# Optimization experiments

Hardware: AMD Instinct MI355X
Metric: run time of the kernel (lower is better)

Reference implementation:

```python
import jax, jax.numpy as jnp
import numpy as np

N_NODES = 100000
N_EDGES = 1000000
F_IN = 32       # CFG.feature_dim
H = 64          # CFG.hidden_dim
H2 = 2 * H      # L1 family: conv1 out = hidden_dim * 2
N_GRAPHS = 64


def gcn_conv(x, src, dst, deg_inv_sqrt, W, b, num_nodes):
    # PyG GCNConv: out = D^{-1/2} (A + I) D^{-1/2} (x @ W) + b
    h = x @ W  # [N, out]
    norm = (deg_inv_sqrt[src] * deg_inv_sqrt[dst])[:, None]  # [E+N, 1]
    msg = h[src] * norm
    return jax.ops.segment_sum(msg, dst, num_segments=num_nodes) + b


def setup_inputs() -> dict:
    key = jax.random.key(0)
    ks = jax.random.split(key, 10)
    x = jax.random.normal(ks[0], (N_NODES, F_IN), dtype=jnp.float32)
    edge_index = jax.random.randint(ks[1], (2, N_EDGES), 0, N_NODES, dtype=jnp.int64)
    batch = jnp.sort(jax.random.randint(ks[2], (N_NODES,), 0, N_GRAPHS, dtype=jnp.int64))
    def glorot(k, shape):
        lim = np.sqrt(6.0 / (shape[0] + shape[1]))
        return jax.random.uniform(k, shape, jnp.float32, -lim, lim)
    W1 = glorot(ks[3], (F_IN, H2))
    b1 = jnp.zeros((H2,), jnp.float32)
    W2 = glorot(ks[4], (H2, H))
    b2 = jnp.zeros((H,), jnp.float32)
    Wrt = glorot(ks[5], (H, H))
    brt = jnp.zeros((H,), jnp.float32)
    return {"x": x, "edge_index": edge_index, "batch": batch,
            "W1": W1, "b1": b1, "W2": W2, "b2": b2, "Wrt": Wrt, "brt": brt}


def reference(x, edge_index, batch, W1, b1, W2, b2, Wrt, brt):
    num_nodes = x.shape[0]
    loop = jnp.arange(num_nodes, dtype=edge_index.dtype)
    src = jnp.concatenate([edge_index[0], loop])  # add self-loops
    dst = jnp.concatenate([edge_index[1], loop])
    deg = jax.ops.segment_sum(jnp.ones_like(dst, dtype=x.dtype), dst, num_segments=num_nodes)
    deg_inv_sqrt = jnp.where(deg > 0, jax.lax.rsqrt(deg), 0.0)

    h = jax.nn.relu(gcn_conv(x, src, dst, deg_inv_sqrt, W1, b1, num_nodes))
    h = gcn_conv(h, src, dst, deg_inv_sqrt, W2, b2, num_nodes)
    h = h @ Wrt + brt  # L1 reverse transcriptase

    # global_mean_pool over batch segments
    sums = jax.ops.segment_sum(h, batch, num_segments=N_GRAPHS)
    counts = jax.ops.segment_sum(jnp.ones((num_nodes,), h.dtype), batch, num_segments=N_GRAPHS)
    pooled = sums / jnp.maximum(counts, 1.0)[:, None]

    activity_factor = 1.0  # age = 0 -> 1/(1+0)
    return pooled * activity_factor
```

## Files before the change

### kernel.cpp

```cpp
#include <hip/hip_runtime.h>

#define NN 100000
#define NE 1000000
#define FIN 32
#define H2 128
#define HH 64
#define NG 64
#define SLOT 16
#define OSLOT 48

#define BSH 9
#define BNODES 512
#define NB 196
#define CAPL 28
#define CAPB 6144
#define CHUNK 2048
#define NSPILL 4096
#define ZN (NN + NG + NG * HH + 256 + 64)

typedef __attribute__((ext_vector_type(8))) short short8;
typedef __attribute__((ext_vector_type(4))) float f32x4;
typedef __attribute__((ext_vector_type(2))) float f32x2;

__device__ __forceinline__ unsigned f2bf(float f) {
    unsigned u = __float_as_uint(f);
    return (u + 0x7FFFu + ((u >> 16) & 1u)) >> 16;
}
__device__ __forceinline__ float bf2f(unsigned u) {
    return __uint_as_float(u << 16);
}
__device__ __forceinline__ void dec8(float* a, float w, uint2 v) {
    f32x2 p0 = __builtin_amdgcn_cvt_pk_f32_fp8((int)v.x, false);
    f32x2 p1 = __builtin_amdgcn_cvt_pk_f32_fp8((int)v.x, true);
    f32x2 p2 = __builtin_amdgcn_cvt_pk_f32_fp8((int)v.y, false);
    f32x2 p3 = __builtin_amdgcn_cvt_pk_f32_fp8((int)v.y, true);
    a[0] = fmaf(w, p0.x, a[0]); a[1] = fmaf(w, p0.y, a[1]);
    a[2] = fmaf(w, p1.x, a[2]); a[3] = fmaf(w, p1.y, a[3]);
    a[4] = fmaf(w, p2.x, a[4]); a[5] = fmaf(w, p2.y, a[5]);
    a[6] = fmaf(w, p3.x, a[6]); a[7] = fmaf(w, p3.y, a[7]);
}
__device__ __forceinline__ unsigned char f2fp8(float f) {
    return (unsigned char)(__builtin_amdgcn_cvt_pk_fp8_f32(f, f, 0, false) & 0xff);
}

__global__ void k_setup(const float* __restrict__ x, const float* __restrict__ W1,
                        const float* __restrict__ W2, const float* __restrict__ Wrt,
                        const float* __restrict__ b2, const float* __restrict__ brt,
                        int* __restrict__ zws, uint2* __restrict__ xb8,
                        unsigned short* __restrict__ w2t, float* __restrict__ brt2,
                        unsigned short* __restrict__ w1t) {
    int i = blockIdx.x * 256 + threadIdx.x;
    if (i < ZN) zws[i] = 0;
    if (i < NN * FIN / 8) {
        float4 a = ((const float4*)x)[2 * i];
        float4 b = ((const float4*)x)[2 * i + 1];
        unsigned u0 = __builtin_amdgcn_cvt_pk_fp8_f32(a.x, a.y, 0, false);
        u0 = __builtin_amdgcn_cvt_pk_fp8_f32(a.z, a.w, u0, true);
        unsigned u1 = __builtin_amdgcn_cvt_pk_fp8_f32(b.x, b.y, 0, false);
        u1 = __builtin_amdgcn_cvt_pk_fp8_f32(b.z, b.w, u1, true);
        xb8[i] = make_uint2(u0, u1);
    }
    if (i < H2 * HH) {
        int r = i >> 6, c = i & 63;
        float acc = 0.f;
        for (int k = 0; k < HH; ++k) acc = fmaf(W2[r * HH + k], Wrt[k * HH + c], acc);
        w2t[c * H2 + r] = (unsigned short)f2bf(acc);
    } else if (i < H2 * HH + HH) {
        int c = i - H2 * HH;
        float acc = brt[c];
        for (int k = 0; k < HH; ++k) acc = fmaf(b2[k], Wrt[k * HH + c], acc);
        brt2[c] = acc;
    } else if (i < H2 * HH + HH + FIN * H2) {
        int j = i - (H2 * HH + HH);
        int k = j >> 7, c = j & 127;
        w1t[c * FIN + k] = (unsigned short)f2bf(W1[j]);
    }
}

__global__ __launch_bounds__(256) void k_bin(const int* __restrict__ ei,
                                             int* __restrict__ gcnt,
                                             unsigned* __restrict__ gbuf,
                                             int* __restrict__ gspillc,
                                             int* __restrict__ gspill) {
    __shared__ int cur[NB];
    __shared__ int gbase[NB];
    __shared__ unsigned stage[NB * CAPL];
    for (int i = threadIdx.x; i < NB; i += 256) cur[i] = 0;
    __syncthreads();
    int e0 = blockIdx.x * CHUNK;
#pragma unroll
    for (int it = 0; it < CHUNK / 256; ++it) {
        int e = e0 + it * 256 + threadIdx.x;
        if (e < NE) {
            int d = ei[NE + e];
            int b = d >> BSH;
            unsigned u = ((unsigned)ei[e] << BSH) | (unsigned)(d & (BNODES - 1));
            int p = atomicAdd(&cur[b], 1);
            if (p < CAPL) stage[b * CAPL + p] = u;
            else {
                int q = atomicAdd(gspillc, 1);
                if (q < NSPILL) { gspill[2 * q] = b; gspill[2 * q + 1] = (int)u; }
            }
        }
    }
    __syncthreads();
    if (threadIdx.x < NB) {
        int len = min(cur[threadIdx.x], CAPL);
        gbase[threadIdx.x] = len ? atomicAdd(&gcnt[threadIdx.x], len) : 0;
    }
    __syncthreads();
    int wid = threadIdx.x >> 6, lane = threadIdx.x & 63;
    for (int b = wid; b < NB; b += 4) {
        int len = min(cur[b], CAPL);
        if (len == 0) continue;
        int base = gbase[b];
        if (base + len > CAPB) len = max(0, CAPB - base);
        if (lane < len)
            gbuf[(size_t)b * CAPB + base + lane] = stage[b * CAPL + lane];
    }
}

__global__ __launch_bounds__(512) void k_build(const unsigned* __restrict__ gbuf,
                                               const int* __restrict__ gcnt,
                                               const int* __restrict__ gspillc,
                                               const int* __restrict__ gspill,
                                               const int* __restrict__ bat,
                                               int* __restrict__ esrc,
                                               int* __restrict__ ovf,
                                               int* __restrict__ fill,
                                               float* __restrict__ dis,
                                               int* __restrict__ counts) {
    __shared__ int cnt[BNODES];
    __shared__ int slots[BNODES * SLOT];
    for (int i = threadIdx.x; i < BNODES; i += 512) cnt[i] = 0;
    __syncthreads();
    int b = blockIdx.x;
    int len = min(gcnt[b], CAPB);
    const unsigned* buf = gbuf + (size_t)b * CAPB;
    for (int i = threadIdx.x; i < len; i += 512) {
        unsigned u = buf[i];
        int ln = u & (BNODES - 1);
        int src = (int)(u >> BSH);
        int p = atomicAdd(&cnt[ln], 1);
        if (p < SLOT) slots[ln * SLOT + p] = src;
        else if (p < SLOT + OSLOT)
            ovf[(size_t)(b * BNODES + ln) * OSLOT + (p - SLOT)] = src;
    }
    int ns = min(*gspillc, NSPILL);
    for (int i = threadIdx.x; i < ns; i += 512) {
        if (gspill[2 * i] == b) {
            unsigned u = (unsigned)gspill[2 * i + 1];
            int ln = u & (BNODES - 1);
            int src = (int)(u >> BSH);
            int p = atomicAdd(&cnt[ln], 1);
            if (p < SLOT) slots[ln * SLOT + p] = src;
            else if (p < SLOT + OSLOT)
                ovf[(size_t)(b * BNODES + ln) * OSLOT + (p - SLOT)] = src;
        }
    }
    __syncthreads();
    int nbase = b * BNODES;
    int nvalid = min(BNODES, NN - nbase);
    if (nvalid <= 0) return;
    {
        int li = threadIdx.x;
        bool v = li < nvalid;
        int n = nbase + li;
        if (v) {
            int c = cnt[li];
            fill[n] = c;
            dis[n] = rsqrtf((float)(c + 1));
        }
        int lane = li & 63;
        int g = v ? bat[n] : -1;
        int gprev = __shfl_up(g, 1, 64);
        bool head = (lane == 0) || (g != gprev);
        unsigned long long hm = __ballot(head && v);
        int gnext = __shfl_down(g, 1, 64);
        bool tail = v && ((lane == 63) || (gnext != g));
        if (tail) {
            unsigned long long below =
                (lane == 63) ? ~0ull : ((1ull << (lane + 1)) - 1ull);
            int start = 63 - __clzll(hm & below);
            atomicAdd(&counts[g], lane - start + 1);
        }
    }
    int nwords = nvalid * SLOT / 4;
    int4* d4 = (int4*)(esrc + (size_t)nbase * SLOT);
    const int4* s4 = (const int4*)slots;
    for (int i = threadIdx.x; i < nwords; i += 512) d4[i] = s4[i];
}

__global__ void k_pack(const int* __restrict__ cnt, const float* __restrict__ dis,
                       int* __restrict__ esrc, int* __restrict__ ovf) {
    int i = blockIdx.x * 256 + threadIdx.x;
    if (i < NN * SLOT) {
        int n = i >> 4, p = i & 15;
        if (p < min(cnt[n], SLOT)) {
            int s = esrc[i];
            esrc[i] = (int)(((unsigned)s << 15) | (f2bf(dis[s]) & 0x7FFFu));
        }
    } else if (i < NN * SLOT + NN) {
        int n = i - NN * SLOT;
        int c = cnt[n];
        if (c > SLOT) {
            int cov = min(c - SLOT, OSLOT);
            int* orow = ovf + (size_t)n * OSLOT;
            for (int q = 0; q < cov; ++q) {
                int s = orow[q];
                orow[q] = (int)(((unsigned)s << 15) | (f2bf(dis[s]) & 0x7FFFu));
            }
        }
    }
}

__global__ __launch_bounds__(256, 4) void k_aggx(
    const uint2* __restrict__ xb8, const float* __restrict__ dis,
    const int* __restrict__ cnt, const int* __restrict__ esrc,
    const int* __restrict__ ovf, uint4* __restrict__ aggx4) {
    int idx = blockIdx.x * 256 + threadIdx.x;
    int n = idx >> 2, t = idx & 3;
    if (n >= NN) return;
    float dn = dis[n];
    float a[8] = {0.f, 0.f, 0.f, 0.f, 0.f, 0.f, 0.f, 0.f};
    dec8(a, dn * dn, xb8[n * 4 + t]);
    int c = cnt[n];
    int c1 = min(c, SLOT);
    if (c1 > 0) {
        const int4* rp = (const int4*)(esrc + (size_t)n * SLOT);
        int4 i0 = rp[0], i1 = rp[1], i2 = rp[2], i3 = rp[3];
        int ej[16] = {i0.x, i0.y, i0.z, i0.w, i1.x, i1.y, i1.z, i1.w,
                      i2.x, i2.y, i2.z, i2.w, i3.x, i3.y, i3.z, i3.w};
        int e0 = i0.x;
#pragma unroll
        for (int j = 0; j < 16; ++j) {
            int e = (j < c1) ? ej[j] : e0;
            int s = (int)((unsigned)e >> 15);
            float w = (j < c1) ? bf2f(e & 0x7FFF) * dn : 0.f;
            dec8(a, w, xb8[(size_t)s * 4 + t]);
        }
    }
    if (c > SLOT) {
        int cov = min(c - SLOT, OSLOT);
        const int* orow = ovf + (size_t)n * OSLOT;
        for (int p = 0; p < cov; ++p) {
            int e = orow[p];
            int s = (int)((unsigned)e >> 15);
            dec8(a, bf2f(e & 0x7FFF) * dn, xb8[(size_t)s * 4 + t]);
        }
    }
    uint4 r;
    r.x = f2bf(a[0]) | (f2bf(a[1]) << 16);
    r.y = f2bf(a[2]) | (f2bf(a[3]) << 16);
    r.z = f2bf(a[4]) | (f2bf(a[5]) << 16);
    r.w = f2bf(a[6]) | (f2bf(a[7]) << 16);
    aggx4[n * 4 + t] = r;
}

__global__ __launch_bounds__(256) void k_mlpm(
    const unsigned short* __restrict__ aggxg, const unsigned short* __restrict__ w1tg,
    const unsigned short* __restrict__ w2tg, const float* __restrict__ b1,
    unsigned char* __restrict__ y) {
    __shared__ unsigned short w1t[H2 * FIN];
    __shared__ unsigned short w2t[HH * H2];
    __shared__ float b1s[H2];
    __shared__ float h1s[4][16 * 132];
    for (int i = threadIdx.x; i < FIN * H2 / 8; i += 256)
        ((uint4*)w1t)[i] = ((const uint4*)w1tg)[i];
    for (int i = threadIdx.x; i < HH * H2 / 8; i += 256)
        ((uint4*)w2t)[i] = ((const uint4*)w2tg)[i];
    if (threadIdx.x < H2) b1s[threadIdx.x] = b1[threadIdx.x];
    __syncthreads();
    int wid = threadIdx.x >> 6, l = threadIdx.x & 63;
    int base = (blockIdx.x * 4 + wid) * 16;
    if (base >= NN) return;
    int lr = l & 15, lk = l >> 4;
    float* h1w = h1s[wid];
    const f32x4 zero = {0.f, 0.f, 0.f, 0.f};

    short8 a1 = ((const short8*)aggxg)[(base + lr) * 4 + lk];
#pragma unroll
    for (int ct = 0; ct < 8; ++ct) {
        short8 bf = *(const short8*)&w1t[(ct * 16 + lr) * FIN + lk * 8];
        f32x4 c = __builtin_amdgcn_mfma_f32_16x16x32_bf16(a1, bf, zero, 0, 0, 0);
        float bv = b1s[ct * 16 + lr];
#pragma unroll
        for (int q = 0; q < 4; ++q)
            h1w[(lk * 4 + q) * 132 + ct * 16 + lr] = fmaxf(c[q] + bv, 0.f);
    }

    f32x4 acc0 = zero, acc1 = zero, acc2 = zero, acc3 = zero;
#pragma unroll
    for (int kt = 0; kt < 4; ++kt) {
        const float* ap = &h1w[lr * 132 + kt * 32 + lk * 8];
        float4 alo = *(const float4*)ap;
        float4 ahi = *(const float4*)(ap + 4);
        short8 af;
        af[0] = (short)f2bf(alo.x); af[1] = (short)f2bf(alo.y);
        af[2] = (short)f2bf(alo.z); af[3] = (short)f2bf(alo.w);
        af[4] = (short)f2bf(ahi.x); af[5] = (short)f2bf(ahi.y);
        af[6] = (short)f2bf(ahi.z); af[7] = (short)f2bf(ahi.w);
        const unsigned short* wb = &w2t[lr * H2 + kt * 32 + lk * 8];
        short8 b0 = *(const short8*)(wb);
        short8 b1f = *(const short8*)(wb + 16 * H2);
        short8 b2f = *(const short8*)(wb + 32 * H2);
        short8 b3f = *(const short8*)(wb + 48 * H2);
        acc0 = __builtin_amdgcn_mfma_f32_16x16x32_bf16(af, b0, acc0, 0, 0, 0);
        acc1 = __builtin_amdgcn_mfma_f32_16x16x32_bf16(af, b1f, acc1, 0, 0, 0);
        acc2 = __builtin_amdgcn_mfma_f32_16x16x32_bf16(af, b2f, acc2, 0, 0, 0);
        acc3 = __builtin_amdgcn_mfma_f32_16x16x32_bf16(af, b3f, acc3, 0, 0, 0);
    }
    unsigned char* ybs = (unsigned char*)h1w;
#pragma unroll
    for (int q = 0; q < 4; ++q) {
        int r = lk * 4 + q;
        ybs[r * 64 + lr +  0] = f2fp8(acc0[q]);
        ybs[r * 64 + lr + 16] = f2fp8(acc1[q]);
        ybs[r * 64 + lr + 32] = f2fp8(acc2[q]);
        ybs[r * 64 + lr + 48] = f2fp8(acc3[q]);
    }
    ((uint4*)(y + (size_t)base * 64))[l] = ((const uint4*)ybs)[l];
}

__global__ __launch_bounds__(256, 4) void k_l2g(
    const uint2* __restrict__ y2, const float* __restrict__ dis,
    const int* __restrict__ cnt, const int* __restrict__ esrc,
    const int* __restrict__ ovf, const float* __restrict__ brt2,
    const int* __restrict__ bat, float* __restrict__ pool) {
    __shared__ float hred[32][HH];
    __shared__ int gids[32];
    int idx = blockIdx.x * 256 + threadIdx.x;
    int n = idx >> 3;
    int t = threadIdx.x & 7;
    int ni = threadIdx.x >> 3;
    float dn = dis[n];
    float a[8];
    {
        float4 blo = ((const float4*)brt2)[t * 2];
        float4 bhi = ((const float4*)brt2)[t * 2 + 1];
        a[0] = blo.x; a[1] = blo.y; a[2] = blo.z; a[3] = blo.w;
        a[4] = bhi.x; a[5] = bhi.y; a[6] = bhi.z; a[7] = bhi.w;
        dec8(a, dn * dn, y2[(size_t)n * 8 + t]);
    }
    int c = cnt[n];
    int c1 = min(c, SLOT);
    if (c1 > 0) {
        const int4* rp = (const int4*)(esrc + (size_t)n * SLOT);
        int4 i0 = rp[0], i1 = rp[1], i2 = rp[2], i3 = rp[3];
        int ej[16] = {i0.x, i0.y, i0.z, i0.w, i1.x, i1.y, i1.z, i1.w,
                      i2.x, i2.y, i2.z, i2.w, i3.x, i3.y, i3.z, i3.w};
        int e0 = i0.x;
#pragma unroll
        for (int j = 0; j < 16; ++j) {
            int e = (j < c1) ? ej[j] : e0;
            int s = (int)((unsigned)e >> 15);
            float w = (j < c1) ? bf2f(e & 0x7FFF) * dn : 0.f;
            dec8(a, w, y2[(size_t)s * 8 + t]);
        }
    }
    if (c > SLOT) {
        int cov = min(c - SLOT, OSLOT);
        const int* orow = ovf + (size_t)n * OSLOT;
        for (int p = 0; p < cov; ++p) {
            int e = orow[p];
            int s = (int)((unsigned)e >> 15);
            dec8(a, bf2f(e & 0x7FFF) * dn, y2[(size_t)s * 8 + t]);
        }
    }
    ((float4*)&hred[ni][t * 8])[0] = make_float4(a[0], a[1], a[2], a[3]);
    ((float4*)&hred[ni][t * 8])[1] = make_float4(a[4], a[5], a[6], a[7]);
    if (t == 0) gids[ni] = bat[n];
    __syncthreads();
    if (threadIdx.x < HH) {
        int f = threadIdx.x;
        int cg = gids[0];
        float s = 0.f;
        for (int j = 0; j < 32; ++j) {
            int g = gids[j];
            if (g != cg) { atomicAdd(&pool[cg * HH + f], s); s = 0.f; cg = g; }
            s += hred[j][f];
        }
        atomicAdd(&pool[cg * HH + f], s);
    }
}

__global__ void k_final(const float* __restrict__ pool, const int* __restrict__ counts,
                        float* __restrict__ out) {
    int i = blockIdx.x * 256 + threadIdx.x;
    if (i < NG * HH) {
        int g = i >> 6;
        out[i] = pool[i] / fmaxf((float)counts[g], 1.0f);
    }
}


extern "C" void kernel_launch(void* const* d_in, const int* in_sizes, int n_in,
                              void* d_out, int out_size, void* d_ws, size_t ws_size,
                              hipStream_t stream) {
    const float* x   = (const float*)d_in[0];
    const int*   ei  = (const int*)d_in[1];
    const int*   bat = (const int*)d_in[2];
    const float* W1  = (const float*)d_in[3];
    const float* b1  = (const float*)d_in[4];
    const float* W2  = (const float*)d_in[5];
    const float* b2  = (const float*)d_in[6];
    const float* Wrt = (const float*)d_in[7];
    const float* brt = (const float*)d_in[8];
    float* out = (float*)d_out;

    int* ws = (int*)d_ws;
    int* fill    = ws;
    int* counts  = ws + NN;
    float* pool  = (float*)(ws + NN + NG);
    int* gcnt    = ws + NN + NG + NG * HH;
    int* gspillc = gcnt + 256;
    int* gspill  = ws + ZN;
    float* dis   = (float*)(gspill + 2 * NSPILL);
    int* esrc    = (int*)dis + NN;
    int* ovf     = esrc + (size_t)NN * SLOT;
    unsigned* gbuf = (unsigned*)(ovf + (size_t)NN * OSLOT);
    uint2* xb8     = (uint2*)(gbuf + (size_t)NB * CAPB);
    unsigned* aggx = (unsigned*)xb8 + NN * 8;
    unsigned char* yb = (unsigned char*)(aggx + NN * 16);
    unsigned short* w1t = (unsigned short*)(yb + (size_t)NN * 64);
    unsigned short* w2t = w1t + FIN * H2;
    float* brt2 = (float*)(w2t + H2 * HH);

    k_setup<<<(NN * FIN / 8 + 255) / 256, 256, 0, stream>>>(
        x, W1, W2, Wrt, b2, brt, ws, xb8, w2t, brt2, w1t);
    k_bin<<<(NE + CHUNK - 1) / CHUNK, 256, 0, stream>>>(ei, gcnt, gbuf, gspillc, gspill);
    k_build<<<NB, 512, 0, stream>>>(gbuf, gcnt, gspillc, gspill, bat,
                                    esrc, ovf, fill, dis, counts);
    k_pack<<<(NN * (SLOT + 1) + 255) / 256, 256, 0, stream>>>(fill, dis, esrc, ovf);
    k_aggx<<<(NN * 4 + 255) / 256, 256, 0, stream>>>(
        xb8, dis, fill, esrc, ovf, (uint4*)aggx);
    k_mlpm<<<(NN + 63) / 64, 256, 0, stream>>>(
        (const unsigned short*)aggx, w1t, w2t, b1, yb);
    k_l2g<<<NN * 8 / 256, 256, 0, stream>>>(
        (const uint2*)yb, dis, fill, esrc, ovf, brt2, bat, pool);
    k_final<<<(NG * HH + 255) / 256, 256, 0, stream>>>(pool, counts, out);
}
```

Measured before the change: 100.9 us.

## Fuse layer-1 gather aggregation into the MLP kernel via shared memory

Merges the per-node neighbor aggregation kernel into the MFMA MLP kernel. Each wavefront aggregates its 16 nodes into LDS and feeds MFMA directly. This removes one kernel launch and the global write/read of the aggregated bf16 features. In exchange, the gather runs at the MLP kernel's occupancy, which is limited by its large LDS footprint, so latency hiding for the random gathers may drop.

```diff
diff --git a/kernel.cpp b/kernel.cpp
--- a/kernel.cpp
+++ b/kernel.cpp
@@ -214,57 +214,17 @@
     }
 }
 
-__global__ __launch_bounds__(256, 4) void k_aggx(
+__global__ __launch_bounds__(256) void k_mlpg(
     const uint2* __restrict__ xb8, const float* __restrict__ dis,
     const int* __restrict__ cnt, const int* __restrict__ esrc,
-    const int* __restrict__ ovf, uint4* __restrict__ aggx4) {
-    int idx = blockIdx.x * 256 + threadIdx.x;
-    int n = idx >> 2, t = idx & 3;
-    if (n >= NN) return;
-    float dn = dis[n];
-    float a[8] = {0.f, 0.f, 0.f, 0.f, 0.f, 0.f, 0.f, 0.f};
-    dec8(a, dn * dn, xb8[n * 4 + t]);
-    int c = cnt[n];
-    int c1 = min(c, SLOT);
-    if (c1 > 0) {
-        const int4* rp = (const int4*)(esrc + (size_t)n * SLOT);
-        int4 i0 = rp[0], i1 = rp[1], i2 = rp[2], i3 = rp[3];
-        int ej[16] = {i0.x, i0.y, i0.z, i0.w, i1.x, i1.y, i1.z, i1.w,
-                      i2.x, i2.y, i2.z, i2.w, i3.x, i3.y, i3.z, i3.w};
-        int e0 = i0.x;
-#pragma unroll
-        for (int j = 0; j < 16; ++j) {
-            int e = (j < c1) ? ej[j] : e0;
-            int s = (int)((unsigned)e >> 15);
-            float w = (j < c1) ? bf2f(e & 0x7FFF) * dn : 0.f;
-            dec8(a, w, xb8[(size_t)s * 4 + t]);
-        }
-    }
-    if (c > SLOT) {
-        int cov = min(c - SLOT, OSLOT);
-        const int* orow = ovf + (size_t)n * OSLOT;
-        for (int p = 0; p < cov; ++p) {
-            int e = orow[p];
-            int s = (int)((unsigned)e >> 15);
-            dec8(a, bf2f(e & 0x7FFF) * dn, xb8[(size_t)s * 4 + t]);
-        }
-    }
-    uint4 r;
-    r.x = f2bf(a[0]) | (f2bf(a[1]) << 16);
-    r.y = f2bf(a[2]) | (f2bf(a[3]) << 16);
-    r.z = f2bf(a[4]) | (f2bf(a[5]) << 16);
-    r.w = f2bf(a[6]) | (f2bf(a[7]) << 16);
-    aggx4[n * 4 + t] = r;
-}
-
-__global__ __launch_bounds__(256) void k_mlpm(
-    const unsigned short* __restrict__ aggxg, const unsigned short* __restrict__ w1tg,
-    const unsigned short* __restrict__ w2tg, const float* __restrict__ b1,
-    unsigned char* __restrict__ y) {
+    const int* __restrict__ ovf,
+    const unsigned short* __restrict__ w1tg, const unsigned short* __restrict__ w2tg,
+    const float* __restrict__ b1, unsigned char* __restrict__ y) {
     __shared__ unsigned short w1t[H2 * FIN];
     __shared__ unsigned short w2t[HH * H2];
     __shared__ float b1s[H2];
     __shared__ float h1s[4][16 * 132];
+    __shared__ __align__(16) unsigned short aggs[4][16 * 40];
     for (int i = threadIdx.x; i < FIN * H2 / 8; i += 256)
         ((uint4*)w1t)[i] = ((const uint4*)w1tg)[i];
     for (int i = threadIdx.x; i < HH * H2 / 8; i += 256)
@@ -274,11 +234,50 @@
     int wid = threadIdx.x >> 6, l = threadIdx.x & 63;
     int base = (blockIdx.x * 4 + wid) * 16;
     if (base >= NN) return;
+
+    {
+        int n = base + (l >> 2), t = l & 3;
+        float dn = dis[n];
+        float a[8] = {0.f, 0.f, 0.f, 0.f, 0.f, 0.f, 0.f, 0.f};
+        dec8(a, dn * dn, xb8[(size_t)n * 4 + t]);
+        int c = cnt[n];
+        int c1 = min(c, SLOT);
+        if (c1 > 0) {
+            const int4* rp = (const int4*)(esrc + (size_t)n * SLOT);
+            int4 i0 = rp[0], i1 = rp[1], i2 = rp[2], i3 = rp[3];
+            int ej[16] = {i0.x, i0.y, i0.z, i0.w, i1.x, i1.y, i1.z, i1.w,
+                          i2.x, i2.y, i2.z, i2.w, i3.x, i3.y, i3.z, i3.w};
+            int e0 = i0.x;
+#pragma unroll
+            for (int j = 0; j < 16; ++j) {
+                int e = (j < c1) ? ej[j] : e0;
+                int s = (int)((unsigned)e >> 15);
+                float w = (j < c1) ? bf2f(e & 0x7FFF) * dn : 0.f;
+                dec8(a, w, xb8[(size_t)s * 4 + t]);
+            }
+        }
+        if (c > SLOT) {
+            int cov = min(c - SLOT, OSLOT);
+            const int* orow = ovf + (size_t)n * OSLOT;
+            for (int p = 0; p < cov; ++p) {
+                int e = orow[p];
+                int s = (int)((unsigned)e >> 15);
+                dec8(a, bf2f(e & 0x7FFF) * dn, xb8[(size_t)s * 4 + t]);
+            }
+        }
+        uint4 r;
+        r.x = f2bf(a[0]) | (f2bf(a[1]) << 16);
+        r.y = f2bf(a[2]) | (f2bf(a[3]) << 16);
+        r.z = f2bf(a[4]) | (f2bf(a[5]) << 16);
+        r.w = f2bf(a[6]) | (f2bf(a[7]) << 16);
+        *(uint4*)(&aggs[wid][(l >> 2) * 40 + t * 8]) = r;
+    }
+
     int lr = l & 15, lk = l >> 4;
     float* h1w = h1s[wid];
     const f32x4 zero = {0.f, 0.f, 0.f, 0.f};
 
-    short8 a1 = ((const short8*)aggxg)[(base + lr) * 4 + lk];
+    short8 a1 = *(const short8*)(&aggs[wid][lr * 40 + lk * 8]);
 #pragma unroll
     for (int ct = 0; ct < 8; ++ct) {
         short8 bf = *(const short8*)&w1t[(ct * 16 + lr) * FIN + lk * 8];
@@ -420,8 +419,7 @@
     int* ovf     = esrc + (size_t)NN * SLOT;
     unsigned* gbuf = (unsigned*)(ovf + (size_t)NN * OSLOT);
     uint2* xb8     = (uint2*)(gbuf + (size_t)NB * CAPB);
-    unsigned* aggx = (unsigned*)xb8 + NN * 8;
-    unsigned char* yb = (unsigned char*)(aggx + NN * 16);
+    unsigned char* yb = (unsigned char*)((unsigned*)xb8 + NN * 8);
     unsigned short* w1t = (unsigned short*)(yb + (size_t)NN * 64);
     unsigned short* w2t = w1t + FIN * H2;
     float* brt2 = (float*)(w2t + H2 * HH);
@@ -432,10 +430,8 @@
     k_build<<<NB, 512, 0, stream>>>(gbuf, gcnt, gspillc, gspill, bat,
                                     esrc, ovf, fill, dis, counts);
     k_pack<<<(NN * (SLOT + 1) + 255) / 256, 256, 0, stream>>>(fill, dis, esrc, ovf);
-    k_aggx<<<(NN * 4 + 255) / 256, 256, 0, stream>>>(
-        xb8, dis, fill, esrc, ovf, (uint4*)aggx);
-    k_mlpm<<<(NN + 63) / 64, 256, 0, stream>>>(
-        (const unsigned short*)aggx, w1t, w2t, b1, yb);
+    k_mlpg<<<(NN + 63) / 64, 256, 0, stream>>>(
+        xb8, dis, fill, esrc, ovf, w1t, w2t, b1, yb);
     k_l2g<<<NN * 8 / 256, 256, 0, stream>>>(
         (const uint2*)yb, dis, fill, esrc, ovf, brt2, bat, pool);
     k_final<<<(NG * HH + 255) / 256, 256, 0, stream>>>(pool, counts, out);
```

Measured after the change: 98.04 us (median of 2 runs). 1.03x faster.
